# Optimization experiments

Hardware: AMD Instinct MI355X
Metric: run time of the kernel (lower is better)

## Reference

```python
import jax, jax.numpy as jnp
import numpy as np

DIM = 1024
HEAD_DIM = 64
N_HEADS = DIM // HEAD_DIM  # 16
COND_DIM = 256
LENGTHS = (1, 4, 16, 64, 256, 1024)
SEQ = sum(LENGTHS)  # 1365
LN_EPS = 1e-5
ROT_D = 3 * (HEAD_DIM // 8)  # 24; 2*ROT_D = 48 <= HEAD_DIM


def _axial_pos(h, w):
    hp = np.linspace(-1.0, 1.0, h + 1); hp = (hp[:-1] + hp[1:]) / 2
    wp = np.linspace(-1.0, 1.0, w + 1); wp = (wp[:-1] + wp[1:]) / 2
    return np.stack(np.meshgrid(hp, wp, indexing='ij'), -1).reshape(h * w, 2)


def _make_theta():
    d = 5
    poses = []
    for i in range(d):
        pa = _axial_pos(32 >> i, 32 >> i)
        pr = np.full((pa.shape[0], 1), (d - i) / d)
        poses.insert(0, np.concatenate([pa, pr], -1))
    poses.insert(0, np.zeros((1, 3)))
    pos = np.concatenate(poses, 0)  # [1365, 3]
    log_min, log_max = np.log(np.pi), np.log(10 * np.pi)
    freqs = np.exp(np.linspace(log_min, log_max, HEAD_DIM // 8 * N_HEADS + 1)[:-1])
    freqs = freqs.reshape(HEAD_DIM // 8, N_HEADS).T  # [H, head_dim//8]
    th = pos[:, None, 0:1] * freqs  # [S, H, head_dim//8]
    tw = pos[:, None, 1:2] * freqs
    td = pos[:, None, 2:3] * freqs
    theta = np.concatenate([th, tw, td], -1)  # [S, H, ROT_D]
    return jnp.asarray(theta.transpose(1, 0, 2), dtype=jnp.float32)  # [H, S, ROT_D]


def _make_mask():
    m = np.zeros((SEQ, SEQ), dtype=bool)
    i = 0
    for L in LENGTHS:
        m[i:, i:i + L] = True
        i += L
    return jnp.asarray(m)


THETA = _make_theta()  # [H, S, ROT_D], constant buffer
MASK = _make_mask()    # [S, S] bool, constant buffer


def _rope(x, theta):
    # x: [B, H, S, head_dim]; theta: [H, S, ROT_D]
    d = theta.shape[-1]
    x1, x2, rest = x[..., :d], x[..., d:2 * d], x[..., 2 * d:]
    cos, sin = jnp.cos(theta), jnp.sin(theta)
    return jnp.concatenate([x1 * cos - x2 * sin, x2 * cos + x1 * sin, rest], -1)


def setup_inputs() -> dict:
    key = jax.random.key(0)
    ks = jax.random.split(key, 6)
    s = 0.02
    x = jax.random.normal(ks[0], (8, SEQ, DIM), jnp.float32)
    cond = jax.random.normal(ks[1], (8, 1, COND_DIM), jnp.float32)
    adaln_w = jax.random.normal(ks[2], (COND_DIM, 2 * DIM), jnp.float32) * s
    adaln_b = jnp.zeros((2 * DIM,), jnp.float32)
    qkv_w = jax.random.normal(ks[3], (DIM, 3 * DIM), jnp.float32) * s
    qkv_b = jnp.zeros((3 * DIM,), jnp.float32)
    out_w = jax.random.normal(ks[4], (DIM, DIM), jnp.float32) * s
    out_b = jnp.zeros((DIM,), jnp.float32)
    return {"x": x, "cond": cond, "adaln_w": adaln_w, "adaln_b": adaln_b,
            "qkv_w": qkv_w, "qkv_b": qkv_b, "out_w": out_w, "out_b": out_b}


def reference(x, cond, adaln_w, adaln_b, qkv_w, qkv_b, out_w, out_b):
    B, S, _ = x.shape
    skip = x
    # AdaLN: zero-init proj in the original; math is LN(x)*(w+1)+b
    wb = cond @ adaln_w + adaln_b  # [B, 1, 2*DIM]
    w, b = jnp.split(wb, 2, axis=-1)
    mu = x.mean(-1, keepdims=True)
    var = ((x - mu) ** 2).mean(-1, keepdims=True)
    xn = (x - mu) * jax.lax.rsqrt(var + LN_EPS)
    xn = xn * (w + 1.0) + b
    # QKV
    qkv = xn @ qkv_w + qkv_b  # [B, S, 3*DIM]
    qkv = qkv.reshape(B, S, 3, N_HEADS, HEAD_DIM).transpose(0, 3, 2, 1, 4)  # [B,H,3,S,hd]
    q, k, v = qkv[:, :, 0], qkv[:, :, 1], qkv[:, :, 2]
    theta = THETA[:, :S]  # [H, S, ROT_D]
    q = _rope(q, theta)
    k = _rope(k, theta)
    # block-causal masked SDPA
    scores = jnp.einsum('bhqd,bhkd->bhqk', q, k) / np.sqrt(HEAD_DIM).astype(np.float32)
    scores = jnp.where(MASK[:S, :S], scores, -1e30)
    attn = jax.nn.softmax(scores, axis=-1)
    o = jnp.einsum('bhqk,bhkd->bhqd', attn, v)
    o = o.transpose(0, 2, 1, 3).reshape(B, S, DIM)
    return o @ out_w + out_b + skip
```

## Files before the change

### kernel.cpp

```cpp
#include <hip/hip_runtime.h>
#include <math.h>


typedef unsigned short u16;
typedef unsigned short u16x8 __attribute__((ext_vector_type(8)));
typedef unsigned short u16x4 __attribute__((ext_vector_type(4)));
typedef __bf16        bf16x8 __attribute__((ext_vector_type(8)));
typedef float         f32x4  __attribute__((ext_vector_type(4)));

#define SEQ  1365
#define SP   1408
#define BHN  128
#define MTOT 10920
#define DIMN 1024
#define QSCALE 0.1803368801111204f

__device__ __forceinline__ u16 f2bf(float x){
  unsigned r; asm("v_cvt_pk_bf16_f32 %0, %1, %1" : "=v"(r) : "v"(x));
  return (u16)r;
}
__device__ __forceinline__ unsigned cvtpk(float a, float b){
  unsigned r; asm("v_cvt_pk_bf16_f32 %0, %1, %2" : "=v"(r) : "v"(a), "v"(b));
  return r;
}
__device__ __forceinline__ float bf2f(u16 b){
  return __builtin_bit_cast(float, ((unsigned)b) << 16);
}
__device__ __forceinline__ bf16x8 ldbf8(const u16* p){
  return __builtin_bit_cast(bf16x8, *(const u16x8*)p);
}
__device__ __forceinline__ bf16x8 ldsv(const char* p){
  return __builtin_bit_cast(bf16x8, *(const u16x8*)p);
}
__device__ __forceinline__ f32x4 mfma16(bf16x8 a, bf16x8 b, f32x4 c){
  return __builtin_amdgcn_mfma_f32_16x16x32_bf16(a, b, c, 0, 0, 0);
}
__device__ __forceinline__ void gload16(const u16* g, u16* l){
  __builtin_amdgcn_global_load_lds(
      (const __attribute__((address_space(1))) void*)(g),
      (__attribute__((address_space(3))) void*)(l), 16, 0, 0);
}

__global__ __launch_bounds__(256) void transpose_bf16(const float* __restrict__ in,
                                                      u16* __restrict__ outT,
                                                      int K, int N){
  __shared__ float tile[32][33];
  const int tx = threadIdx.x & 31, ty = threadIdx.x >> 5;
  const int n0 = blockIdx.x*32, k0 = blockIdx.y*32;
#pragma unroll
  for (int i=0;i<32;i+=8) tile[ty+i][tx] = in[(size_t)(k0+ty+i)*N + n0+tx];
  __syncthreads();
#pragma unroll
  for (int i=0;i<32;i+=8) outT[(size_t)(n0+ty+i)*K + k0+tx] = f2bf(tile[tx][ty+i]);
}

__global__ __launch_bounds__(256) void adaln_kernel(const float* __restrict__ cond,
                                                    const float* __restrict__ w,
                                                    const float* __restrict__ bsrc,
                                                    float* __restrict__ wb){
  __shared__ float cs[256];
  const int bt = blockIdx.x >> 3, ch = blockIdx.x & 7;
  const int t = threadIdx.x;
  cs[t] = cond[bt*256 + t];
  __syncthreads();
  const int n = ch*256 + t;
  float acc = bsrc[n];
  for (int j=0;j<256;j++) acc += cs[j] * w[(size_t)j*2048 + n];
  wb[bt*2048 + n] = acc;
}

__global__ __launch_bounds__(256) void theta_kernel(float* __restrict__ ctab,
                                                    float* __restrict__ stab){
  int idx = blockIdx.x*256 + threadIdx.x;
  if (idx >= 16*SEQ*24) return;
  int c = idx % 24;
  int rest = idx / 24;
  int s = rest % SEQ;
  int h = rest / SEQ;
  float p0 = 0.f, p1 = 0.f, p2 = 0.f;
  if (s >= 1){
    int start, sh; float pr;
    if      (s <   5){start=1;   sh=1; pr=0.2f;}
    else if (s <  21){start=5;   sh=2; pr=0.4f;}
    else if (s <  85){start=21;  sh=3; pr=0.6f;}
    else if (s < 341){start=85;  sh=4; pr=0.8f;}
    else             {start=341; sh=5; pr=1.0f;}
    int n = s - start;
    int row = n >> sh, colp = n & ((1<<sh)-1);
    float g = (float)(1 << sh);
    p0 = -1.f + (2*row+1)/g;
    p1 = -1.f + (2*colp+1)/g;
    p2 = pr;
  }
  int j = c & 7, comp = c >> 3;
  float kf = (float)(j*16 + h);
  float freq = 3.14159265358979323846f * exp2f(kf * (3.3219280948873623f/128.f));
  float pos = (comp==0) ? p0 : ((comp==1) ? p1 : p2);
  float th = pos * freq;
  ctab[idx] = cosf(th);
  stab[idx] = sinf(th);
}

__global__ __launch_bounds__(256) void ln_kernel(const float* __restrict__ x,
                                                 const float* __restrict__ wb,
                                                 u16* __restrict__ xn){
  const int row = blockIdx.x;
  const int b = row / SEQ;
  const int t = threadIdx.x, w = t>>6, l = t&63;
  const float4 v = ((const float4*)(x + (size_t)row*DIMN))[t];
  float s = v.x + v.y + v.z + v.w;
#pragma unroll
  for (int m=1; m<64; m<<=1) s += __shfl_xor(s, m);
  __shared__ float red1[4], red2[4];
  if (l == 0) red1[w] = s;
  __syncthreads();
  float mean = (red1[0]+red1[1]+red1[2]+red1[3]) * (1.f/1024.f);
  float dx = v.x-mean, dy = v.y-mean, dz = v.z-mean, dw = v.w-mean;
  float q = dx*dx + dy*dy + dz*dz + dw*dw;
#pragma unroll
  for (int m=1; m<64; m<<=1) q += __shfl_xor(q, m);
  if (l == 0) red2[w] = q;
  __syncthreads();
  float var = (red2[0]+red2[1]+red2[2]+red2[3]) * (1.f/1024.f);
  float rs = rsqrtf(var + 1e-5f);
  const float* wrow = wb + b*2048;
  int n0 = t*4;
  u16x4 o;
  o[0] = f2bf(dx*rs*(wrow[n0+0]+1.f) + wrow[1024+n0+0]);
  o[1] = f2bf(dy*rs*(wrow[n0+1]+1.f) + wrow[1024+n0+1]);
  o[2] = f2bf(dz*rs*(wrow[n0+2]+1.f) + wrow[1024+n0+2]);
  o[3] = f2bf(dw*rs*(wrow[n0+3]+1.f) + wrow[1024+n0+3]);
  *(u16x4*)&xn[(size_t)row*DIMN + n0] = o;
}

#define GSTAGE(dstA, dstB, koff)                                   \
  do {                                                             \
    _Pragma("unroll")                                              \
    for (int j_=0;j_<4;j_++) gload16(sA[j_]+(koff), (dstA)+j_*512);\
    _Pragma("unroll")                                              \
    for (int j_=0;j_<4;j_++) gload16(sB[j_]+(koff), (dstB)+j_*512);\
  } while(0)

__global__ __launch_bounds__(256, 2) void gemm_qkv(const u16* __restrict__ A,
                                                   const u16* __restrict__ BT,
                                                   const float* __restrict__ bias,
                                                   u16* __restrict__ qb, u16* __restrict__ kb,
                                                   u16* __restrict__ vb){
  __shared__ u16 As[2][8192];
  __shared__ u16 Bs[2][8192];
  const int t = threadIdx.x, l = t & 63, w = t >> 6;
  const int lr = l & 15, lg = l >> 4;
  const int wr = w >> 1, wc = w & 1;

  const int bid = blockIdx.x;
  const int wg = (bid & 7)*258 + (bid >> 3);
  const int stile = wg/96, rr = wg - stile*96;
  const int mt = stile*4 + rr/24, nt = rr - (rr/24)*24;
  const int bm = mt*128, bn = nt*128;

  const int row8 = l >> 3;
  const int gch  = (l & 7) ^ row8;
  const u16* sA[4]; const u16* sB[4];
#pragma unroll
  for (int j=0;j<4;j++){
    int gr = bm + w*32 + j*8 + row8; if (gr >= MTOT) gr = MTOT-1;
    sA[j] = A  + (size_t)gr*1024 + gch*8;
    sB[j] = BT + (size_t)(bn + w*32 + j*8 + row8)*1024 + gch*8;
  }
  u16* dA0 = &As[0][w*2048]; u16* dB0 = &Bs[0][w*2048];
  u16* dA1 = &As[1][w*2048]; u16* dB1 = &Bs[1][w*2048];

  const int pch  = (lg ^ (lr & 7)) << 4;
  const int aoff = (wr*64 + lr)*128 + pch;
  const int boff = (wc*64 + lr)*128 + pch;

  f32x4 acc[4][4];
#pragma unroll
  for (int mi=0;mi<4;mi++)
#pragma unroll
    for (int ni=0;ni<4;ni++) acc[mi][ni] = (f32x4){0.f,0.f,0.f,0.f};

  GSTAGE(dA0, dB0, 0);
  GSTAGE(dA1, dB1, 64);
  asm volatile("s_waitcnt vmcnt(8)" ::: "memory");
  __builtin_amdgcn_s_barrier();
  __builtin_amdgcn_sched_barrier(0);

  for (int kt = 0; kt < 16; ++kt){
    const int bi = kt & 1;
    const char* Ab = (const char*)As[bi];
    const char* Bb = (const char*)Bs[bi];
    u16* dA = bi ? dA1 : dA0;
    u16* dB = bi ? dB1 : dB0;
    bf16x8 a0[4], b0[4], a1[4], b1[4];
#pragma unroll
    for (int mi=0;mi<4;mi++) a0[mi] = ldsv(Ab + (aoff + mi*2048));
#pragma unroll
    for (int ni=0;ni<4;ni++) b0[ni] = ldsv(Bb + (boff + ni*2048));
#pragma unroll
    for (int mi=0;mi<4;mi++) a1[mi] = ldsv(Ab + ((aoff + mi*2048) ^ 64));
#pragma unroll
    for (int ni=0;ni<4;ni++) b1[ni] = ldsv(Bb + ((boff + ni*2048) ^ 64));
    __builtin_amdgcn_s_setprio(1);
#pragma unroll
    for (int mi=0;mi<4;mi++)
#pragma unroll
      for (int ni=0;ni<4;ni++)
        acc[mi][ni] = mfma16(a0[mi], b0[ni], acc[mi][ni]);
    __builtin_amdgcn_s_setprio(0);
    asm volatile("s_waitcnt lgkmcnt(0)" ::: "memory");
    __builtin_amdgcn_s_barrier();
    __builtin_amdgcn_sched_barrier(0);
    if (kt < 14) GSTAGE(dA, dB, (kt+2)*64);
    __builtin_amdgcn_sched_barrier(0);
    __builtin_amdgcn_s_setprio(1);
#pragma unroll
    for (int mi=0;mi<4;mi++)
#pragma unroll
      for (int ni=0;ni<4;ni++)
        acc[mi][ni] = mfma16(a1[mi], b1[ni], acc[mi][ni]);
    __builtin_amdgcn_s_setprio(0);
    if (kt < 15){
      if (kt < 14) asm volatile("s_waitcnt vmcnt(8)" ::: "memory");
      else         asm volatile("s_waitcnt vmcnt(0)" ::: "memory");
      __builtin_amdgcn_s_barrier();
      __builtin_amdgcn_sched_barrier(0);
    }
  }

#pragma unroll
  for (int mi=0;mi<4;mi++)
#pragma unroll
    for (int ni=0;ni<4;ni++){
      int col = bn + wc*64 + ni*16 + lr;
      float bia = bias[col];
      int three = col >> 10, rem = col & 1023;
      int h = rem >> 6, d = rem & 63;
      float scl = (three == 0) ? QSCALE : 1.0f;
#pragma unroll
      for (int r=0;r<4;r++){
        int m = bm + wr*64 + mi*16 + lg*4 + r;
        if (m < MTOT){
          int b = m / SEQ; int s = m - b*SEQ;
          u16 val = f2bf((acc[mi][ni][r] + bia) * scl);
          int bh = b*16 + h;
          if (three == 0)      qb[((size_t)bh*SP + s)*64 + d] = val;
          else if (three == 1) kb[((size_t)bh*SP + s)*64 + d] = val;
          else                 vb[((size_t)bh*64 + d)*SP + s] = val;
        }
      }
    }
}

__global__ __launch_bounds__(256) void rope2_kernel(u16* __restrict__ qb,
                                                    u16* __restrict__ kb,
                                                    const float* __restrict__ ctab,
                                                    const float* __restrict__ stab){
  int rid = blockIdx.x*256 + threadIdx.x;
  if (rid >= BHN*SEQ) return;
  int bh = rid / SEQ, s = rid - bh*SEQ, h = bh & 15;
  const float* cp = ctab + (size_t)(h*SEQ + s)*24;
  const float* sp = stab + (size_t)(h*SEQ + s)*24;
  float cs[24], sn[24];
#pragma unroll
  for (int i=0;i<6;i++){
    ((float4*)cs)[i] = ((const float4*)cp)[i];
    ((float4*)sn)[i] = ((const float4*)sp)[i];
  }
  size_t base = ((size_t)bh*SP + s)*64;
  u16 buf[48];
#pragma unroll
  for (int i=0;i<6;i++) ((u16x8*)buf)[i] = *(const u16x8*)&qb[base + i*8];
#pragma unroll
  for (int j=0;j<24;j++){
    float x1 = bf2f(buf[j]), x2 = bf2f(buf[24+j]);
    buf[j]    = f2bf(x1*cs[j] - x2*sn[j]);
    buf[24+j] = f2bf(x2*cs[j] + x1*sn[j]);
  }
#pragma unroll
  for (int i=0;i<6;i++) *(u16x8*)&qb[base + i*8] = ((u16x8*)buf)[i];
#pragma unroll
  for (int i=0;i<6;i++) ((u16x8*)buf)[i] = *(const u16x8*)&kb[base + i*8];
#pragma unroll
  for (int j=0;j<24;j++){
    float x1 = bf2f(buf[j]), x2 = bf2f(buf[24+j]);
    buf[j]    = f2bf(x1*cs[j] - x2*sn[j]);
    buf[24+j] = f2bf(x2*cs[j] + x1*sn[j]);
  }
#pragma unroll
  for (int i=0;i<6;i++) *(u16x8*)&kb[base + i*8] = ((u16x8*)buf)[i];
}

__global__ __launch_bounds__(256) void attn_kernel(const u16* __restrict__ qb,
                                                   const u16* __restrict__ kb,
                                                   const u16* __restrict__ vb,
                                                   u16* __restrict__ ob){
  __shared__ u16 Ks[64*72];
  __shared__ u16 Vs[64*72];
  __shared__ u16 Ps[128*72];
  const int bx = blockIdx.x;
  const int qt = (bx < 9) ? (bx + 2) : (bx - 9);
  const int bh = blockIdx.y;
  const int t = threadIdx.x, w = t>>6, l = t&63, lr = l&15, lg = l>>4, lg4 = lg<<2;
  const u16* qB = qb + (size_t)bh*SP*64;
  const u16* kB = kb + (size_t)bh*SP*64;
  const u16* vB = vb + (size_t)bh*64*SP;
  const int q0 = qt*128 + w*32;

  bf16x8 qf[2][2];
#pragma unroll
  for (int ni=0; ni<2; ni++)
#pragma unroll
    for (int kk=0; kk<2; kk++)
      qf[ni][kk] = ldbf8(&qB[(size_t)(q0+ni*16+lr)*64 + kk*32 + lg*8]);
  const int qg0 = q0 + lr, qg1 = q0 + 16 + lr;

  f32x4 oacc[2][4];
#pragma unroll
  for (int mo=0;mo<2;mo++)
#pragma unroll
    for (int nd=0;nd<4;nd++) oacc[mo][nd] = (f32x4){0.f,0.f,0.f,0.f};
  float lst[2] = {0.f, 0.f};

  int qmax = min(qt*128+127, SEQ-1);
  int kend = (qmax<1)?1:(qmax<5)?5:(qmax<21)?21:(qmax<85)?85:(qmax<341)?341:SEQ;
  int nkt = (kend + 63) >> 6;

  for (int kt=0; kt<nkt; kt++){
    const int kbase = kt*64;
    __syncthreads();
#pragma unroll
    for (int j=0;j<2;j++){
      int flat = t + j*256;
      int row = flat >> 3, kc = (flat & 7) << 3;
      *(u16x8*)&Ks[row*72+kc] = *(const u16x8*)&kB[(size_t)(kbase+row)*64 + kc];
      *(u16x8*)&Vs[row*72+kc] = *(const u16x8*)&vB[(size_t)row*SP + kbase + kc];
    }
    __syncthreads();

    f32x4 sacc[4][2];
#pragma unroll
    for (int mi=0;mi<4;mi++){
      sacc[mi][0] = (f32x4){0.f,0.f,0.f,0.f};
      sacc[mi][1] = (f32x4){0.f,0.f,0.f,0.f};
    }
#pragma unroll
    for (int mi=0;mi<4;mi++){
      bf16x8 k0f = ldbf8(&Ks[(mi*16+lr)*72 + lg*8]);
      bf16x8 k1f = ldbf8(&Ks[(mi*16+lr)*72 + 32 + lg*8]);
      sacc[mi][0] = mfma16(k0f, qf[0][0], sacc[mi][0]);
      sacc[mi][0] = mfma16(k1f, qf[0][1], sacc[mi][0]);
      sacc[mi][1] = mfma16(k0f, qf[1][0], sacc[mi][1]);
      sacc[mi][1] = mfma16(k1f, qf[1][1], sacc[mi][1]);
    }

    int lastk = kbase + 63;
    int visLast = (lastk>=SEQ)?(1<<30):(lastk>=341)?341:(lastk>=85)?85:
                  (lastk>=21)?21:(lastk>=5)?5:(lastk>=1)?1:0;
    if (visLast > q0){
#pragma unroll
      for (int mi=0;mi<4;mi++){
        int kv = kbase + mi*16 + lg4;
#pragma unroll
        for (int r=0;r<4;r++){
          int key = kv + r;
          int visv = (key>=SEQ)?(1<<30):(key>=341)?341:(key>=85)?85:
                     (key>=21)?21:(key>=5)?5:(key>=1)?1:0;
          if (qg0 < visv) sacc[mi][0][r] = -1e30f;
          if (qg1 < visv) sacc[mi][1][r] = -1e30f;
        }
      }
    }

    float pa[2] = {0.f, 0.f}, pb[2] = {0.f, 0.f};
#pragma unroll
    for (int mi=0;mi<4;mi++)
#pragma unroll
      for (int ni=0;ni<2;ni++){
        float p0 = __builtin_amdgcn_exp2f(sacc[mi][ni][0]);
        float p1 = __builtin_amdgcn_exp2f(sacc[mi][ni][1]);
        float p2 = __builtin_amdgcn_exp2f(sacc[mi][ni][2]);
        float p3 = __builtin_amdgcn_exp2f(sacc[mi][ni][3]);
        pa[ni] += p0 + p1;
        pb[ni] += p2 + p3;
        uint2 pk = { cvtpk(p0, p1), cvtpk(p2, p3) };
        *(uint2*)&Ps[(w*32+ni*16+lr)*72 + mi*16 + lg4] = pk;
      }
#pragma unroll
    for (int ni=0;ni<2;ni++){
      float s = pa[ni] + pb[ni];
      s += __shfl_xor(s, 16);
      s += __shfl_xor(s, 32);
      lst[ni] += s;
    }

    bf16x8 pf[2][2];
#pragma unroll
    for (int mo=0;mo<2;mo++)
#pragma unroll
      for (int kk=0;kk<2;kk++)
        pf[mo][kk] = ldbf8(&Ps[(w*32+mo*16+lr)*72 + kk*32 + lg*8]);
#pragma unroll
    for (int nd=0;nd<4;nd++){
      bf16x8 v0 = ldbf8(&Vs[(nd*16+lr)*72 + lg*8]);
      bf16x8 v1 = ldbf8(&Vs[(nd*16+lr)*72 + 32 + lg*8]);
#pragma unroll
      for (int mo=0;mo<2;mo++){
        oacc[mo][nd] = mfma16(pf[mo][0], v0, oacc[mo][nd]);
        oacc[mo][nd] = mfma16(pf[mo][1], v1, oacc[mo][nd]);
      }
    }
  }

  const int b = bh >> 4, h = bh & 15;
  float linv[2][4];
#pragma unroll
  for (int mo=0;mo<2;mo++)
#pragma unroll
    for (int r=0;r<4;r++)
      linv[mo][r] = 1.f / __shfl(lst[mo], lg4 + r);
#pragma unroll
  for (int mo=0;mo<2;mo++)
#pragma unroll
    for (int r=0;r<4;r++){
      int p = q0 + mo*16 + lg4 + r;
      if (p < SEQ){
#pragma unroll
        for (int nd=0;nd<4;nd++)
          ob[((size_t)(b*SEQ + p))*DIMN + h*64 + nd*16 + lr] = f2bf(oacc[mo][nd][r] * linv[mo][r]);
      }
    }
}

__global__ __launch_bounds__(256, 2) void gemm_out(const u16* __restrict__ A,
                                                   const u16* __restrict__ BT,
                                                   const float* __restrict__ bias,
                                                   const float* __restrict__ skip,
                                                   float* __restrict__ out){
  __shared__ u16 As[2][8192];
  __shared__ u16 Bs[2][8192];
  const int t = threadIdx.x, l = t & 63, w = t >> 6;
  const int lr = l & 15, lg = l >> 4;
  const int wr = w >> 1, wc = w & 1;

  const int bid = blockIdx.x;
  const int wg = (bid & 7)*86 + (bid >> 3);
  const int stile = wg/32, rr = wg - stile*32;
  const int mt = stile*4 + rr/8, nt = rr & 7;
  const int bm = mt*128, bn = nt*128;

  const int row8 = l >> 3;
  const int gch  = (l & 7) ^ row8;
  const u16* sA[4]; const u16* sB[4];
#pragma unroll
  for (int j=0;j<4;j++){
    int gr = bm + w*32 + j*8 + row8; if (gr >= MTOT) gr = MTOT-1;
    sA[j] = A  + (size_t)gr*1024 + gch*8;
    sB[j] = BT + (size_t)(bn + w*32 + j*8 + row8)*1024 + gch*8;
  }
  u16* dA0 = &As[0][w*2048]; u16* dB0 = &Bs[0][w*2048];
  u16* dA1 = &As[1][w*2048]; u16* dB1 = &Bs[1][w*2048];

  const int pch  = (lg ^ (lr & 7)) << 4;
  const int aoff = (wr*64 + lr)*128 + pch;
  const int boff = (wc*64 + lr)*128 + pch;

  f32x4 acc[4][4];
#pragma unroll
  for (int mi=0;mi<4;mi++)
#pragma unroll
    for (int ni=0;ni<4;ni++) acc[mi][ni] = (f32x4){0.f,0.f,0.f,0.f};

  GSTAGE(dA0, dB0, 0);
  GSTAGE(dA1, dB1, 64);
  asm volatile("s_waitcnt vmcnt(8)" ::: "memory");
  __builtin_amdgcn_s_barrier();
  __builtin_amdgcn_sched_barrier(0);

  for (int kt = 0; kt < 16; ++kt){
    const int bi = kt & 1;
    const char* Ab = (const char*)As[bi];
    const char* Bb = (const char*)Bs[bi];
    u16* dA = bi ? dA1 : dA0;
    u16* dB = bi ? dB1 : dB0;
    bf16x8 a0[4], b0[4], a1[4], b1[4];
#pragma unroll
    for (int mi=0;mi<4;mi++) a0[mi] = ldsv(Ab + (aoff + mi*2048));
#pragma unroll
    for (int ni=0;ni<4;ni++) b0[ni] = ldsv(Bb + (boff + ni*2048));
#pragma unroll
    for (int mi=0;mi<4;mi++) a1[mi] = ldsv(Ab + ((aoff + mi*2048) ^ 64));
#pragma unroll
    for (int ni=0;ni<4;ni++) b1[ni] = ldsv(Bb + ((boff + ni*2048) ^ 64));
    __builtin_amdgcn_s_setprio(1);
#pragma unroll
    for (int mi=0;mi<4;mi++)
#pragma unroll
      for (int ni=0;ni<4;ni++)
        acc[mi][ni] = mfma16(a0[mi], b0[ni], acc[mi][ni]);
    __builtin_amdgcn_s_setprio(0);
    asm volatile("s_waitcnt lgkmcnt(0)" ::: "memory");
    __builtin_amdgcn_s_barrier();
    __builtin_amdgcn_sched_barrier(0);
    if (kt < 14) GSTAGE(dA, dB, (kt+2)*64);
    __builtin_amdgcn_sched_barrier(0);
    __builtin_amdgcn_s_setprio(1);
#pragma unroll
    for (int mi=0;mi<4;mi++)
#pragma unroll
      for (int ni=0;ni<4;ni++)
        acc[mi][ni] = mfma16(a1[mi], b1[ni], acc[mi][ni]);
    __builtin_amdgcn_s_setprio(0);
    if (kt < 15){
      if (kt < 14) asm volatile("s_waitcnt vmcnt(8)" ::: "memory");
      else         asm volatile("s_waitcnt vmcnt(0)" ::: "memory");
      __builtin_amdgcn_s_barrier();
      __builtin_amdgcn_sched_barrier(0);
    }
  }

#pragma unroll
  for (int mi=0;mi<4;mi++)
#pragma unroll
    for (int ni=0;ni<4;ni++){
      int col = bn + wc*64 + ni*16 + lr;
      float bia = bias[col];
#pragma unroll
      for (int r=0;r<4;r++){
        int m = bm + wr*64 + mi*16 + lg*4 + r;
        if (m < MTOT){
          size_t idx2 = (size_t)m*DIMN + col;
          out[idx2] = acc[mi][ni][r] + bia + skip[idx2];
        }
      }
    }
}

extern "C" void kernel_launch(void* const* d_in, const int* in_sizes, int n_in,
                              void* d_out, int out_size, void* d_ws, size_t ws_size,
                              hipStream_t stream) {
  (void)in_sizes; (void)n_in; (void)out_size; (void)ws_size;
  const float* x        = (const float*)d_in[0];
  const float* cond     = (const float*)d_in[1];
  const float* adaln_w  = (const float*)d_in[2];
  const float* adaln_b  = (const float*)d_in[3];
  const float* qkv_w    = (const float*)d_in[4];
  const float* qkv_b    = (const float*)d_in[5];
  const float* out_w    = (const float*)d_in[6];
  const float* out_b    = (const float*)d_in[7];
  float* out = (float*)d_out;

  char* ws = (char*)d_ws;
  size_t off = 0;
  auto alloc = [&](size_t bytes)->void*{
    void* p = ws + off;
    off += (bytes + 255) & ~(size_t)255;
    return p;
  };
  float* wb     = (float*)alloc((size_t)8*2048*4);
  u16*   xn     = (u16*)  alloc((size_t)MTOT*DIMN*2);
  u16*   qkv_wT = (u16*)  alloc((size_t)3072*1024*2);
  u16*   out_wT = (u16*)  alloc((size_t)1024*1024*2);
  u16*   qbuf   = (u16*)  alloc((size_t)BHN*SP*64*2);
  u16*   kbuf   = (u16*)  alloc((size_t)BHN*SP*64*2);
  u16*   vbuf   = (u16*)  alloc((size_t)BHN*SP*64*2);
  float* ctab   = (float*)alloc((size_t)16*SEQ*24*4);
  float* stab   = (float*)alloc((size_t)16*SEQ*24*4);
  u16*   obuf   = xn;

  transpose_bf16<<<dim3(3072/32, 1024/32), 256, 0, stream>>>(qkv_w, qkv_wT, 1024, 3072);
  transpose_bf16<<<dim3(1024/32, 1024/32), 256, 0, stream>>>(out_w, out_wT, 1024, 1024);
  theta_kernel<<<(16*SEQ*24 + 255)/256, 256, 0, stream>>>(ctab, stab);
  adaln_kernel<<<64, 256, 0, stream>>>(cond, adaln_w, adaln_b, wb);
  ln_kernel<<<MTOT, 256, 0, stream>>>(x, wb, xn);
  gemm_qkv<<<2064, 256, 0, stream>>>(xn, qkv_wT, qkv_b, qbuf, kbuf, vbuf);
  rope2_kernel<<<(BHN*SEQ + 255)/256, 256, 0, stream>>>(qbuf, kbuf, ctab, stab);
  attn_kernel<<<dim3((SEQ+127)/128, BHN), 256, 0, stream>>>(qbuf, kbuf, vbuf, obuf);
  gemm_out<<<688, 256, 0, stream>>>(obuf, out_wT, out_b, x, out);
}
```

Measured before the change: 452.8 us.

## Stage GEMM epilogues through LDS for coalesced vector stores, per-batch M tiling

Both GEMMs now tile M per batch, 11 tiles of 128 rows per sequence, so each tile stays inside one batch. The QKV epilogue writes results into shared memory and then issues coalesced 16-byte stores to the q/k layout and to the transposed v layout, replacing scattered 2-byte stores. The output GEMM stages fp32 results in LDS and does float4 skip-add stores. This adds padded tiles (2112/704 blocks instead of 2064/688) plus extra barriers and LDS traffic, in exchange for much better global store coalescing.

```diff
diff --git a/kernel.cpp b/kernel.cpp
--- a/kernel.cpp
+++ b/kernel.cpp
@@ -146,29 +146,32 @@
                                                    const float* __restrict__ bias,
                                                    u16* __restrict__ qb, u16* __restrict__ kb,
                                                    u16* __restrict__ vb){
-  __shared__ u16 As[2][8192];
-  __shared__ u16 Bs[2][8192];
+  __shared__ u16 SMEM[32768];
+  u16* As0 = SMEM;        u16* As1 = SMEM + 8192;
+  u16* Bs0 = SMEM + 16384; u16* Bs1 = SMEM + 24576;
   const int t = threadIdx.x, l = t & 63, w = t >> 6;
   const int lr = l & 15, lg = l >> 4;
   const int wr = w >> 1, wc = w & 1;
 
   const int bid = blockIdx.x;
-  const int wg = (bid & 7)*258 + (bid >> 3);
+  const int wg = (bid & 7)*264 + (bid >> 3);
   const int stile = wg/96, rr = wg - stile*96;
   const int mt = stile*4 + rr/24, nt = rr - (rr/24)*24;
-  const int bm = mt*128, bn = nt*128;
+  const int bat = mt / 11, mtl = mt - bat*11;
+  const int s0 = mtl*128;
+  const int bn = nt*128;
 
   const int row8 = l >> 3;
   const int gch  = (l & 7) ^ row8;
   const u16* sA[4]; const u16* sB[4];
 #pragma unroll
   for (int j=0;j<4;j++){
-    int gr = bm + w*32 + j*8 + row8; if (gr >= MTOT) gr = MTOT-1;
-    sA[j] = A  + (size_t)gr*1024 + gch*8;
+    int srow = s0 + w*32 + j*8 + row8; if (srow > SEQ-1) srow = SEQ-1;
+    sA[j] = A  + ((size_t)(bat*SEQ + srow))*1024 + gch*8;
     sB[j] = BT + (size_t)(bn + w*32 + j*8 + row8)*1024 + gch*8;
   }
-  u16* dA0 = &As[0][w*2048]; u16* dB0 = &Bs[0][w*2048];
-  u16* dA1 = &As[1][w*2048]; u16* dB1 = &Bs[1][w*2048];
+  u16* dA0 = &As0[w*2048]; u16* dB0 = &Bs0[w*2048];
+  u16* dA1 = &As1[w*2048]; u16* dB1 = &Bs1[w*2048];
 
   const int pch  = (lg ^ (lr & 7)) << 4;
   const int aoff = (wr*64 + lr)*128 + pch;
@@ -188,8 +191,8 @@
 
   for (int kt = 0; kt < 16; ++kt){
     const int bi = kt & 1;
-    const char* Ab = (const char*)As[bi];
-    const char* Bb = (const char*)Bs[bi];
+    const char* Ab = (const char*)(bi ? As1 : As0);
+    const char* Bb = (const char*)(bi ? Bs1 : Bs0);
     u16* dA = bi ? dA1 : dA0;
     u16* dB = bi ? dB1 : dB0;
     bf16x8 a0[4], b0[4], a1[4], b1[4];
@@ -228,28 +231,72 @@
     }
   }
 
-#pragma unroll
-  for (int mi=0;mi<4;mi++)
-#pragma unroll
-    for (int ni=0;ni<4;ni++){
-      int col = bn + wc*64 + ni*16 + lr;
-      float bia = bias[col];
-      int three = col >> 10, rem = col & 1023;
-      int h = rem >> 6, d = rem & 63;
-      float scl = (three == 0) ? QSCALE : 1.0f;
-#pragma unroll
-      for (int r=0;r<4;r++){
-        int m = bm + wr*64 + mi*16 + lg*4 + r;
-        if (m < MTOT){
-          int b = m / SEQ; int s = m - b*SEQ;
-          u16 val = f2bf((acc[mi][ni][r] + bia) * scl);
-          int bh = b*16 + h;
-          if (three == 0)      qb[((size_t)bh*SP + s)*64 + d] = val;
-          else if (three == 1) kb[((size_t)bh*SP + s)*64 + d] = val;
-          else                 vb[((size_t)bh*64 + d)*SP + s] = val;
+  __syncthreads();
+  const int three = bn >> 10;
+  const int hb = (bn & 1023) >> 6;
+  if (three < 2){
+    const float scl = (three==0) ? QSCALE : 1.0f;
+#pragma unroll
+    for (int mi=0;mi<4;mi++)
+#pragma unroll
+      for (int ni=0;ni<4;ni++){
+        int col = wc*64 + ni*16 + lr;
+        float bia = bias[bn + col];
+#pragma unroll
+        for (int r=0;r<4;r++){
+          int ml = wr*64 + mi*16 + lg*4 + r;
+          SMEM[ml*136 + col] = f2bf((acc[mi][ni][r] + bia) * scl);
         }
       }
-    }
+    __syncthreads();
+    u16* dst = (three==0) ? qb : kb;
+    const int cs = t & 15, tm = t >> 4;
+    const int h = hb + (cs>>3), d8 = (cs&7)*8;
+#pragma unroll
+    for (int p=0;p<8;p++){
+      int ml = p*16 + tm;
+      int s = s0 + ml;
+      u16x8 vv = *(const u16x8*)&SMEM[ml*136 + cs*8];
+      if (s < SEQ)
+        *(u16x8*)&dst[((size_t)(bat*16 + h)*SP + s)*64 + d8] = vv;
+    }
+  } else {
+#pragma unroll
+    for (int mi=0;mi<4;mi++)
+#pragma unroll
+      for (int ni=0;ni<4;ni++){
+        int col = wc*64 + ni*16 + lr;
+        float bia = bias[bn + col];
+#pragma unroll
+        for (int r=0;r<4;r+=2){
+          int ml = wr*64 + mi*16 + lg*4 + r;
+          *(unsigned*)&SMEM[col*136 + ml] = cvtpk(acc[mi][ni][r]+bia, acc[mi][ni][r+1]+bia);
+        }
+      }
+    __syncthreads();
+    const int ss = t & 15, tdl = t >> 4;
+    if (s0 + 127 < SEQ){
+#pragma unroll
+      for (int p=0;p<8;p++){
+        int dl = p*16 + tdl;
+        int h = hb + (dl>>6), d = dl & 63;
+        u16x8 vv = *(const u16x8*)&SMEM[dl*136 + ss*8];
+        *(u16x8*)&vb[((size_t)(bat*16 + h)*64 + d)*SP + s0 + ss*8] = vv;
+      }
+    } else {
+#pragma unroll
+      for (int p=0;p<8;p++){
+        int dl = p*16 + tdl;
+        int h = hb + (dl>>6), d = dl & 63;
+        size_t rowb = ((size_t)(bat*16 + h)*64 + d)*SP;
+#pragma unroll
+        for (int j=0;j<8;j++){
+          int s = s0 + ss*8 + j;
+          if (s < SEQ) vb[rowb + s] = SMEM[dl*136 + ss*8 + j];
+        }
+      }
+    }
+  }
 }
 
 __global__ __launch_bounds__(256) void rope2_kernel(u16* __restrict__ qb,
@@ -437,29 +484,32 @@
                                                    const float* __restrict__ bias,
                                                    const float* __restrict__ skip,
                                                    float* __restrict__ out){
-  __shared__ u16 As[2][8192];
-  __shared__ u16 Bs[2][8192];
+  __shared__ u16 SMEM[32768];
+  u16* As0 = SMEM;        u16* As1 = SMEM + 8192;
+  u16* Bs0 = SMEM + 16384; u16* Bs1 = SMEM + 24576;
   const int t = threadIdx.x, l = t & 63, w = t >> 6;
   const int lr = l & 15, lg = l >> 4;
   const int wr = w >> 1, wc = w & 1;
 
   const int bid = blockIdx.x;
-  const int wg = (bid & 7)*86 + (bid >> 3);
-  const int stile = wg/32, rr = wg - stile*32;
+  const int wg = (bid & 7)*88 + (bid >> 3);
+  const int stile = wg/32, rr = wg & 31;
   const int mt = stile*4 + rr/8, nt = rr & 7;
-  const int bm = mt*128, bn = nt*128;
+  const int bat = mt / 11, mtl = mt - bat*11;
+  const int s0 = mtl*128;
+  const int bn = nt*128;
 
   const int row8 = l >> 3;
   const int gch  = (l & 7) ^ row8;
   const u16* sA[4]; const u16* sB[4];
 #pragma unroll
   for (int j=0;j<4;j++){
-    int gr = bm + w*32 + j*8 + row8; if (gr >= MTOT) gr = MTOT-1;
-    sA[j] = A  + (size_t)gr*1024 + gch*8;
+    int srow = s0 + w*32 + j*8 + row8; if (srow > SEQ-1) srow = SEQ-1;
+    sA[j] = A  + ((size_t)(bat*SEQ + srow))*1024 + gch*8;
     sB[j] = BT + (size_t)(bn + w*32 + j*8 + row8)*1024 + gch*8;
   }
-  u16* dA0 = &As[0][w*2048]; u16* dB0 = &Bs[0][w*2048];
-  u16* dA1 = &As[1][w*2048]; u16* dB1 = &Bs[1][w*2048];
+  u16* dA0 = &As0[w*2048]; u16* dB0 = &Bs0[w*2048];
+  u16* dA1 = &As1[w*2048]; u16* dB1 = &Bs1[w*2048];
 
   const int pch  = (lg ^ (lr & 7)) << 4;
   const int aoff = (wr*64 + lr)*128 + pch;
@@ -479,8 +529,8 @@
 
   for (int kt = 0; kt < 16; ++kt){
     const int bi = kt & 1;
-    const char* Ab = (const char*)As[bi];
-    const char* Bb = (const char*)Bs[bi];
+    const char* Ab = (const char*)(bi ? As1 : As0);
+    const char* Bb = (const char*)(bi ? Bs1 : Bs0);
     u16* dA = bi ? dA1 : dA0;
     u16* dB = bi ? dB1 : dB0;
     bf16x8 a0[4], b0[4], a1[4], b1[4];
@@ -519,21 +569,34 @@
     }
   }
 
+  __syncthreads();
+  float* Lf = (float*)SMEM;
 #pragma unroll
   for (int mi=0;mi<4;mi++)
 #pragma unroll
     for (int ni=0;ni<4;ni++){
-      int col = bn + wc*64 + ni*16 + lr;
-      float bia = bias[col];
+      int col = wc*64 + ni*16 + lr;
+      float bia = bias[bn + col];
 #pragma unroll
       for (int r=0;r<4;r++){
-        int m = bm + wr*64 + mi*16 + lg*4 + r;
-        if (m < MTOT){
-          size_t idx2 = (size_t)m*DIMN + col;
-          out[idx2] = acc[mi][ni][r] + bia + skip[idx2];
-        }
-      }
-    }
+        int ml = wr*64 + mi*16 + lg*4 + r;
+        Lf[ml*128 + col] = acc[mi][ni][r] + bia;
+      }
+    }
+  __syncthreads();
+  const int cs = t & 31, tm = t >> 5;
+#pragma unroll
+  for (int p=0;p<16;p++){
+    int ml = p*8 + tm;
+    int s = s0 + ml;
+    if (s < SEQ){
+      size_t idx2 = (size_t)(bat*SEQ + s)*1024 + bn + cs*4;
+      float4 v4 = *(const float4*)&Lf[ml*128 + cs*4];
+      const float4 sk = *(const float4*)&skip[idx2];
+      float4 o4; o4.x=v4.x+sk.x; o4.y=v4.y+sk.y; o4.z=v4.z+sk.z; o4.w=v4.w+sk.w;
+      *(float4*)&out[idx2] = o4;
+    }
+  }
 }
 
 extern "C" void kernel_launch(void* const* d_in, const int* in_sizes, int n_in,
@@ -573,8 +636,8 @@
   theta_kernel<<<(16*SEQ*24 + 255)/256, 256, 0, stream>>>(ctab, stab);
   adaln_kernel<<<64, 256, 0, stream>>>(cond, adaln_w, adaln_b, wb);
   ln_kernel<<<MTOT, 256, 0, stream>>>(x, wb, xn);
-  gemm_qkv<<<2064, 256, 0, stream>>>(xn, qkv_wT, qkv_b, qbuf, kbuf, vbuf);
+  gemm_qkv<<<2112, 256, 0, stream>>>(xn, qkv_wT, qkv_b, qbuf, kbuf, vbuf);
   rope2_kernel<<<(BHN*SEQ + 255)/256, 256, 0, stream>>>(qbuf, kbuf, ctab, stab);
   attn_kernel<<<dim3((SEQ+127)/128, BHN), 256, 0, stream>>>(qbuf, kbuf, vbuf, obuf);
-  gemm_out<<<688, 256, 0, stream>>>(obuf, out_wT, out_b, x, out);
-}
+  gemm_out<<<704, 256, 0, stream>>>(obuf, out_wT, out_b, x, out);
+}
```

Measured after the change: 393.8 us. 1.15x faster.
